# Kernel optimization log

Measured on AMD Instinct MI355X. Metric: run time of the kernel, lower is better.

The kernel has to match this reference:

```python
import jax, jax.numpy as jnp
import numpy as np

DZ, H, DH = 128, 4, 32
DC = H * DH
B, L, N = 1, 256, 256


def setup_inputs() -> dict:
    key = jax.random.key(0)
    ks = jax.random.split(key, 12)
    s = 0.02
    return {
        "z_inter": jax.random.normal(ks[0], (B, L, N, DZ), jnp.float32),
        "dist": jax.random.uniform(ks[1], (B, L, N, N), jnp.float32) * 16.0,
        "ln_g": jnp.ones((DZ,), jnp.float32),
        "ln_b": jnp.zeros((DZ,), jnp.float32),
        "Wq": jax.random.normal(ks[2], (DZ, DC), jnp.float32) * s,
        "bq": jnp.zeros((DC,), jnp.float32),
        "Wk": jax.random.normal(ks[3], (DZ, DC), jnp.float32) * s,
        "bk": jnp.zeros((DC,), jnp.float32),
        "Wv": jax.random.normal(ks[4], (DZ, DC), jnp.float32) * s,
        "bv": jnp.zeros((DC,), jnp.float32),
        "Wg": jax.random.normal(ks[5], (DZ, DC), jnp.float32) * s,
        "bg": jnp.zeros((DC,), jnp.float32),
        "Wo": jax.random.normal(ks[6], (DC, DZ), jnp.float32) * s,
        "bo": jnp.zeros((DZ,), jnp.float32),
    }


def reference(z_inter, dist, ln_g, ln_b, Wq, bq, Wk, bk, Wv, bv, Wg, bg, Wo, bo):
    # LayerNorm over channel dim (eps matches torch default 1e-5)
    mu = jnp.mean(z_inter, axis=-1, keepdims=True)
    var = jnp.mean(jnp.square(z_inter - mu), axis=-1, keepdims=True)
    z = (z_inter - mu) / jnp.sqrt(var + 1e-5) * ln_g + ln_b  # [B,L,N,DZ]

    shp = z.shape[:-1] + (H, DH)
    q = (z @ Wq + bq).reshape(shp)  # [B,L,N,H,DH]
    k = (z @ Wk + bk).reshape(shp)
    v = (z @ Wv + bv).reshape(shp)

    scalar = 1.0 / jnp.sqrt(jnp.asarray(DH, q.dtype))
    attn = jnp.einsum('blihc,bljhc->blihj', q * scalar, k)  # [B,L,N,H,N]

    # Gaussian distance coefficient applied multiplicatively pre-softmax
    coef = jnp.exp(-jnp.square(dist / 8.0) / 2.0)[:, :, :, None, :].astype(q.dtype)
    attn = attn * coef

    attn_weights = jax.nn.softmax(attn, axis=-1)
    v_avg = jnp.einsum('blihj,bljhc->blihc', attn_weights, v)  # [B,L,N,H,DH]

    gate = jax.nn.sigmoid((z @ Wg + bg).reshape(shp))
    z_com = (v_avg * gate).reshape(z.shape[:-1] + (DC,))  # [B,L,N,DC]
    return z_com @ Wo + bo  # [B,L,N,DZ]
```

## Files before the change

### kernel.cpp

```cpp
#include <hip/hip_runtime.h>
#include <hip/hip_fp16.h>

#define LDIM 256
#define NDIM 256
#define DZC  128
#define HN   4
#define DHD  32
#define DCC  128
#define MROWS (LDIM*NDIM)

typedef _Float16 f16;
typedef _Float16 f16x2 __attribute__((ext_vector_type(2)));
typedef _Float16 f16x4 __attribute__((ext_vector_type(4)));
typedef _Float16 f16x8 __attribute__((ext_vector_type(8)));
typedef __fp16   h16x2 __attribute__((ext_vector_type(2)));
typedef float    f32x4 __attribute__((ext_vector_type(4)));

#define SCAL 0.17677669529663687f
#define CEXP -0.011270992135622957f
#define CPRE 0.2550340490960039f

extern "C" __device__ _Float16 __ocml_exp2_f16(_Float16);

__device__ inline f16x2 pkrtz(float a, float b){
  h16x2 r = __builtin_amdgcn_cvt_pkrtz(a, b);
  union { h16x2 h; f16x2 f; } u; u.h = r;
  return u.f;
}

__global__ __launch_bounds__(256) void k0b_pack(
    const float* __restrict__ Wq, const float* __restrict__ Wk,
    const float* __restrict__ Wv, const float* __restrict__ Wg,
    const float* __restrict__ Wo, f16* __restrict__ w16)
{
  const float* Ws[5] = {Wq, Wk, Wv, Wg, Wo};
  const int tid = blockIdx.x * 256 + threadIdx.x;
  const int p = tid >> 14, rem = tid & 16383;
  const int e = rem & 7, lane = (rem >> 3) & 63, ksjt = rem >> 9;
  const int ks = ksjt & 3, jt = ksjt >> 2;
  const int col = jt*16 + (lane & 15);
  const int k   = ks*32 + (lane >> 4)*8 + e;
  w16[tid] = (f16)Ws[p][k*128 + col];
}

__global__ __launch_bounds__(256, 2) void k1_ln_qkvg(
    const float* __restrict__ z, const float* __restrict__ lng, const float* __restrict__ lnb,
    const f16* __restrict__ w16,
    const float* __restrict__ bq, const float* __restrict__ bk,
    const float* __restrict__ bv, const float* __restrict__ bg,
    f16* __restrict__ qb, f16* __restrict__ kbuf,
    f16* __restrict__ vbuf, f16* __restrict__ gateb)
{
  __shared__ f16 sb[4*32*136];
  f16* zl = sb;
  const int t = threadIdx.x;
  const int w = t >> 6, lane = t & 63;
  const int m = lane & 15, g = lane >> 4;
  const int row0 = blockIdx.x * 32;

  {
    const int r = t >> 3, part = t & 7;
    const float* zr = z + (size_t)(row0 + r)*DZC + part*16;
    float vals[16];
    float s = 0.f, sq = 0.f;
    #pragma unroll
    for (int i = 0; i < 4; ++i) {
      float4 v4 = reinterpret_cast<const float4*>(zr)[i];
      vals[i*4+0]=v4.x; vals[i*4+1]=v4.y; vals[i*4+2]=v4.z; vals[i*4+3]=v4.w;
      s  += v4.x+v4.y+v4.z+v4.w;
      sq += v4.x*v4.x + v4.y*v4.y + v4.z*v4.z + v4.w*v4.w;
    }
    s  += __shfl_xor(s, 1);  sq += __shfl_xor(sq, 1);
    s  += __shfl_xor(s, 2);  sq += __shfl_xor(sq, 2);
    s  += __shfl_xor(s, 4);  sq += __shfl_xor(sq, 4);
    const float mu  = s * (1.f/DZC);
    const float var = sq * (1.f/DZC) - mu*mu;
    const float rstd = rsqrtf(var + 1e-5f);
    const float* gg = lng + part*16;
    const float* bb = lnb + part*16;
    #pragma unroll
    for (int i = 0; i < 2; ++i) {
      f16x8 o;
      #pragma unroll
      for (int e = 0; e < 8; ++e)
        o[e] = (f16)((vals[i*8+e]-mu)*rstd*gg[i*8+e] + bb[i*8+e]);
      *reinterpret_cast<f16x8*>(zl + r*128 + (((part*2+i) ^ (r&7))*8)) = o;
    }
  }
  __syncthreads();

  const f16* wp = w16 + w*16384;
  f32x4 acc[2][8];
  #pragma unroll
  for (int it=0;it<2;++it)
    #pragma unroll
    for (int jt=0;jt<8;++jt) acc[it][jt] = (f32x4){0.f,0.f,0.f,0.f};

  #pragma unroll
  for (int ks = 0; ks < 4; ++ks) {
    f16x8 af[8];
    #pragma unroll
    for (int jt=0;jt<8;++jt)
      af[jt] = *reinterpret_cast<const f16x8*>(wp + ((jt*4+ks)*64 + lane)*8);
    f16x8 bf[2];
    #pragma unroll
    for (int it=0;it<2;++it)
      bf[it] = *reinterpret_cast<const f16x8*>(zl + (it*16+m)*128 + (((ks*4+g) ^ (m&7))*8));
    #pragma unroll
    for (int it=0;it<2;++it)
      #pragma unroll
      for (int jt=0;jt<8;++jt)
        acc[it][jt] = __builtin_amdgcn_mfma_f32_16x16x32_f16(af[jt], bf[it], acc[it][jt], 0,0,0);
  }

  const float* bsp = (w==0) ? bq : (w==1) ? bk : (w==2) ? bv : bg;
  float4 bias[8];
  #pragma unroll
  for (int jt=0;jt<8;++jt)
    bias[jt] = *reinterpret_cast<const float4*>(bsp + jt*16 + g*4);

  __syncthreads();

  f16* tl = sb + w*(32*136);
  #pragma unroll
  for (int it=0;it<2;++it) {
    #pragma unroll
    for (int jt=0;jt<8;++jt) {
      f16x4 o;
      #pragma unroll
      for (int r=0;r<4;++r) {
        float v = acc[it][jt][r] + ((const float*)&bias[jt])[r];
        if (w == 3) v = 1.f/(1.f + __expf(-v));
        o[r] = (f16)v;
      }
      *reinterpret_cast<f16x4*>(tl + (it*16+m)*136 + jt*16 + g*4) = o;
    }
  }
  f16* ob = (w==0) ? qb : (w==1) ? kbuf : (w==2) ? vbuf : gateb;
  #pragma unroll
  for (int p = 0; p < 8; ++p) {
    const int rr = p*4 + g, cc = m*8;
    const f16x8 v = *reinterpret_cast<const f16x8*>(tl + rr*136 + cc);
    *reinterpret_cast<f16x8*>(ob + (size_t)(row0 + rr)*DCC + cc) = v;
  }
}

__global__ __launch_bounds__(256, 2) void k2_attn(
    const f16* __restrict__ qb, const f16* __restrict__ kbuf,
    const f16* __restrict__ vbuf, const f16* __restrict__ gateb,
    const float* __restrict__ dist, const f16* __restrict__ wo16,
    const float* __restrict__ bo, float* __restrict__ out)
{
  __shared__ f16 vt[4*32*256];
  __shared__ f16 cfl[2][64*64];
  const int t = threadIdx.x;
  const int w = t >> 6, lane = t & 63;
  const int m = lane & 15, g = lane >> 4;
  const int orig = blockIdx.x;
  const int swz = (orig & 7)*64 + (orig >> 3);
  const int l = swz >> 1, half = swz & 1;
  const int r0 = half*128;
  const int lrow0 = l*NDIM;

  {
    #pragma unroll
    for (int hh = 0; hh < 4; ++hh) {
      const f16* vr = vbuf + (size_t)(lrow0 + t)*DCC + hh*DHD;
      #pragma unroll
      for (int p = 0; p < 4; ++p) {
        f16x8 v = *reinterpret_cast<const f16x8*>(vr + p*8);
        #pragma unroll
        for (int e = 0; e < 8; ++e) {
          const int c = p*8 + e;
          vt[hh*8192 + c*256 + (((t>>2) ^ (c&15))*4) + (t&3)] = v[e];
        }
      }
    }
  }

  f16x8 aq[8];
  #pragma unroll
  for (int it = 0; it < 8; ++it)
    aq[it] = *reinterpret_cast<const f16x8*>(
        qb + (size_t)(lrow0 + r0 + it*16 + m)*DCC + w*DHD + g*8);

  f32x4 o[8][2];
  float rs[8];
  #pragma unroll
  for (int it = 0; it < 8; ++it) {
    o[it][0] = (f32x4){0.f,0.f,0.f,0.f};
    o[it][1] = (f32x4){0.f,0.f,0.f,0.f};
    rs[it] = 0.f;
  }

  const float* drow = dist + (size_t)l*(NDIM*NDIM);
  const int prow[4] = { (0*256+t) >> 4, (1*256+t) >> 4, (2*256+t) >> 4, (3*256+t) >> 4 };
  const int pf4  = t & 15;

  float4 pf[4];
  #pragma unroll
  for (int p = 0; p < 4; ++p)
    pf[p] = *reinterpret_cast<const float4*>(
        drow + (size_t)(r0 + prow[p])*NDIM + pf4*4);

  __syncthreads();

  const f16* vth = vt + w*8192;

  #pragma unroll 1
  for (int jc = 0; jc < 4; ++jc) {
    f16x8 kf[4];
    #pragma unroll
    for (int jt = 0; jt < 4; ++jt)
      kf[jt] = *reinterpret_cast<const f16x8*>(
          kbuf + (size_t)(lrow0 + jc*64 + jt*16 + m)*DCC + w*DHD + g*8);

    f16x8 bvv[2][2];
    #pragma unroll
    for (int kc = 0; kc < 2; ++kc)
      #pragma unroll
      for (int ct = 0; ct < 2; ++ct) {
        const int c = ct*16 + m;
        const f16x4 lo = *reinterpret_cast<const f16x4*>(
            vth + c*256 + (((jc*16 + (2*kc+0)*4 + g) ^ m) * 4));
        const f16x4 hi = *reinterpret_cast<const f16x4*>(
            vth + c*256 + (((jc*16 + (2*kc+1)*4 + g) ^ m) * 4));
        f16x8 bb;
        #pragma unroll
        for (int e = 0; e < 4; ++e) { bb[e] = lo[e]; bb[4+e] = hi[e]; }
        bvv[kc][ct] = bb;
      }

    #pragma unroll
    for (int rh = 0; rh < 2; ++rh) {
      f16* cflc = &cfl[rh][0];
      {
        const float4 dd[4] = {pf[0], pf[1], pf[2], pf[3]};
        #pragma unroll
        for (int p = 0; p < 4; ++p) {
          const int row = prow[p];
          const f16x2 a = pkrtz(CPRE*exp2f(dd[p].x*dd[p].x*CEXP),
                                CPRE*exp2f(dd[p].y*dd[p].y*CEXP));
          const f16x2 b = pkrtz(CPRE*exp2f(dd[p].z*dd[p].z*CEXP),
                                CPRE*exp2f(dd[p].w*dd[p].w*CEXP));
          const f16x4 cf = __builtin_shufflevector(a, b, 0,1,2,3);
          *reinterpret_cast<f16x4*>(cflc + row*64 + ((pf4 ^ (row & 15))*4)) = cf;
        }
      }
      {
        const int si1 = jc*2 + rh + 1;
        const int sic = (si1 > 7) ? 7 : si1;
        const int jn = sic >> 1, rn = sic & 1;
        #pragma unroll
        for (int p = 0; p < 4; ++p)
          pf[p] = *reinterpret_cast<const float4*>(
              drow + (size_t)(r0 + rn*64 + prow[p])*NDIM + jn*64 + pf4*4);
      }
      __syncthreads();

      #pragma unroll
      for (int itl = 0; itl < 4; ++itl) {
        const int it = rh*4 + itl;
        const int lr = itl*16 + m;
        f16x4 cl[4];
        #pragma unroll
        for (int jt = 0; jt < 4; ++jt)
          cl[jt] = *reinterpret_cast<const f16x4*>(
              cflc + lr*64 + (((jt*4 + g) ^ m)*4));

        f32x4 s[4];
        #pragma unroll
        for (int jt = 0; jt < 4; ++jt)
          s[jt] = __builtin_amdgcn_mfma_f32_16x16x32_f16(
              kf[jt], aq[it], (f32x4){0.f,0.f,0.f,0.f}, 0, 0, 0);

        f16x4 pkk[4];
        #pragma unroll
        for (int jt = 0; jt < 4; ++jt) {
          const f16x2 sl = pkrtz(s[jt][0], s[jt][1]);
          const f16x2 sh = pkrtz(s[jt][2], s[jt][3]);
          const f16x2 cll = __builtin_shufflevector(cl[jt], cl[jt], 0,1);
          const f16x2 clh = __builtin_shufflevector(cl[jt], cl[jt], 2,3);
          const f16x2 xl = sl * cll;
          const f16x2 xh = sh * clh;
          f16x4 pv;
          pv[0] = __ocml_exp2_f16(xl[0]);
          pv[1] = __ocml_exp2_f16(xl[1]);
          pv[2] = __ocml_exp2_f16(xh[0]);
          pv[3] = __ocml_exp2_f16(xh[1]);
          pkk[jt] = pv;
        }
        {
          const f16x4 ps4 = (pkk[0] + pkk[1]) + (pkk[2] + pkk[3]);
          const f16x2 ps2 = __builtin_shufflevector(ps4, ps4, 0,1)
                          + __builtin_shufflevector(ps4, ps4, 2,3);
          rs[it] += (float)ps2[0] + (float)ps2[1];
        }

        #pragma unroll
        for (int kc = 0; kc < 2; ++kc) {
          const f16x8 ap = __builtin_shufflevector(pkk[2*kc], pkk[2*kc+1],
                                                   0,1,2,3,4,5,6,7);
          o[it][0] = __builtin_amdgcn_mfma_f32_16x16x32_f16(ap, bvv[kc][0], o[it][0], 0, 0, 0);
          o[it][1] = __builtin_amdgcn_mfma_f32_16x16x32_f16(ap, bvv[kc][1], o[it][1], 0, 0, 0);
        }
      }
    }
  }

  float rinv[8];
  #pragma unroll
  for (int it = 0; it < 8; ++it) {
    float v = rs[it];
    v += __shfl_xor(v, 16);
    v += __shfl_xor(v, 32);
    rinv[it] = 1.f / v;
  }

  __syncthreads();
  f16* zc = vt;
  #pragma unroll
  for (int it = 0; it < 8; ++it)
    #pragma unroll
    for (int r = 0; r < 4; ++r) {
      const float rr = __shfl(rinv[it], (lane & 48) + g*4 + r);
      const int lrow = it*16 + g*4 + r;
      #pragma unroll
      for (int ct = 0; ct < 2; ++ct)
        zc[lrow*132 + w*DHD + ct*16 + m] = (f16)(o[it][ct][r] * rr);
    }
  __syncthreads();

  f32x4 acc2[2][8];
  #pragma unroll
  for (int it2=0;it2<2;++it2)
    #pragma unroll
    for (int jt=0;jt<8;++jt) acc2[it2][jt] = (f32x4){0.f,0.f,0.f,0.f};

  #pragma unroll
  for (int ks = 0; ks < 4; ++ks) {
    f16x8 af[8];
    #pragma unroll
    for (int jt=0;jt<8;++jt)
      af[jt] = *reinterpret_cast<const f16x8*>(wo16 + ((jt*4+ks)*64 + lane)*8);
    f16x8 bf[2];
    #pragma unroll
    for (int it2 = 0; it2 < 2; ++it2) {
      const int lrow = w*32 + it2*16 + m;
      const f16x4 b0 = *reinterpret_cast<const f16x4*>(zc + lrow*132 + ks*32 + g*8);
      const f16x4 b1 = *reinterpret_cast<const f16x4*>(zc + lrow*132 + ks*32 + g*8 + 4);
      const f16x8 zf = __builtin_shufflevector(b0, b1, 0,1,2,3,4,5,6,7);
      const f16x8 gf = *reinterpret_cast<const f16x8*>(
          gateb + (size_t)(lrow0 + r0 + lrow)*DCC + ks*32 + g*8);
      bf[it2] = zf * gf;
    }
    #pragma unroll
    for (int it2=0;it2<2;++it2)
      #pragma unroll
      for (int jt=0;jt<8;++jt)
        acc2[it2][jt] = __builtin_amdgcn_mfma_f32_16x16x32_f16(af[jt], bf[it2], acc2[it2][jt], 0,0,0);
  }

  #pragma unroll
  for (int it2 = 0; it2 < 2; ++it2) {
    const size_t grow = (size_t)(lrow0 + r0 + w*32 + it2*16 + m);
    #pragma unroll
    for (int jt = 0; jt < 8; ++jt) {
      const float4 bias = *reinterpret_cast<const float4*>(bo + jt*16 + g*4);
      float4 ov;
      ov.x = acc2[it2][jt][0] + bias.x;
      ov.y = acc2[it2][jt][1] + bias.y;
      ov.z = acc2[it2][jt][2] + bias.z;
      ov.w = acc2[it2][jt][3] + bias.w;
      *reinterpret_cast<float4*>(out + grow*DZC + jt*16 + g*4) = ov;
    }
  }
}

extern "C" void kernel_launch(void* const* d_in, const int* in_sizes, int n_in,
                              void* d_out, int out_size, void* d_ws, size_t ws_size,
                              hipStream_t stream) {
  const float* z    = (const float*)d_in[0];
  const float* dist = (const float*)d_in[1];
  const float* lng  = (const float*)d_in[2];
  const float* lnb  = (const float*)d_in[3];
  const float* Wq   = (const float*)d_in[4];
  const float* bq   = (const float*)d_in[5];
  const float* Wk   = (const float*)d_in[6];
  const float* bk   = (const float*)d_in[7];
  const float* Wv   = (const float*)d_in[8];
  const float* bv   = (const float*)d_in[9];
  const float* Wg   = (const float*)d_in[10];
  const float* bg   = (const float*)d_in[11];
  const float* Wo   = (const float*)d_in[12];
  const float* bo   = (const float*)d_in[13];
  float* out = (float*)d_out;

  const size_t elems = (size_t)MROWS * DCC;
  f16* qb    = (f16*)d_ws;
  f16* kbuf  = qb    + elems;
  f16* vbuf  = kbuf  + elems;
  f16* gateb = vbuf  + elems;
  f16* w16   = gateb + elems;

  k0b_pack<<<320, 256, 0, stream>>>(Wq, Wk, Wv, Wg, Wo, w16);
  k1_ln_qkvg<<<MROWS/32, 256, 0, stream>>>(z, lng, lnb, w16, bq, bk, bv, bg,
                                           qb, kbuf, vbuf, gateb);
  k2_attn<<<LDIM*2, 256, 0, stream>>>(qb, kbuf, vbuf, gateb, dist,
                                      w16 + 4*16384, bo, out);
}
```

Before: 76.88 us.

## Compute softmax row sums via MFMA with ones and prefetch next K chunk

The per-row softmax denominator was built from packed f16 adds, a float accumulation and cross-lane shuffles. It is now produced by an extra MFMA that multiplies the probability tile by a vector of ones, which yields the row sums already in output-fragment layout. This removes the VALU reduction and the shuffle-based broadcast of the reciprocal. K fragments for the next column chunk are also loaded one iteration early, so that global load latency overlaps compute. The cost is 50% more MFMAs in the PV stage and extra registers for the accumulators and the prefetched fragments, which may reduce occupancy.

```diff
diff --git a/kernel.cpp b/kernel.cpp
--- a/kernel.cpp
+++ b/kernel.cpp
@@ -184,13 +184,17 @@
     aq[it] = *reinterpret_cast<const f16x8*>(
         qb + (size_t)(lrow0 + r0 + it*16 + m)*DCC + w*DHD + g*8);
 
+  f16x8 ones;
+  #pragma unroll
+  for (int e = 0; e < 8; ++e) ones[e] = (f16)1.0f;
+
   f32x4 o[8][2];
-  float rs[8];
+  f32x4 rsacc[8];
   #pragma unroll
   for (int it = 0; it < 8; ++it) {
     o[it][0] = (f32x4){0.f,0.f,0.f,0.f};
     o[it][1] = (f32x4){0.f,0.f,0.f,0.f};
-    rs[it] = 0.f;
+    rsacc[it] = (f32x4){0.f,0.f,0.f,0.f};
   }
 
   const float* drow = dist + (size_t)l*(NDIM*NDIM);
@@ -202,6 +206,11 @@
   for (int p = 0; p < 4; ++p)
     pf[p] = *reinterpret_cast<const float4*>(
         drow + (size_t)(r0 + prow[p])*NDIM + pf4*4);
+  f16x8 kfc[4];
+  #pragma unroll
+  for (int jt = 0; jt < 4; ++jt)
+    kfc[jt] = *reinterpret_cast<const f16x8*>(
+        kbuf + (size_t)(lrow0 + jt*16 + m)*DCC + w*DHD + g*8);
 
   __syncthreads();
 
@@ -209,11 +218,14 @@
 
   #pragma unroll 1
   for (int jc = 0; jc < 4; ++jc) {
-    f16x8 kf[4];
-    #pragma unroll
-    for (int jt = 0; jt < 4; ++jt)
-      kf[jt] = *reinterpret_cast<const f16x8*>(
-          kbuf + (size_t)(lrow0 + jc*64 + jt*16 + m)*DCC + w*DHD + g*8);
+    f16x8 kfn[4];
+    {
+      const int jn2 = (jc + 1 > 3) ? 3 : jc + 1;
+      #pragma unroll
+      for (int jt = 0; jt < 4; ++jt)
+        kfn[jt] = *reinterpret_cast<const f16x8*>(
+            kbuf + (size_t)(lrow0 + jn2*64 + jt*16 + m)*DCC + w*DHD + g*8);
+    }
 
     f16x8 bvv[2][2];
     #pragma unroll
@@ -272,7 +284,7 @@
         #pragma unroll
         for (int jt = 0; jt < 4; ++jt)
           s[jt] = __builtin_amdgcn_mfma_f32_16x16x32_f16(
-              kf[jt], aq[it], (f32x4){0.f,0.f,0.f,0.f}, 0, 0, 0);
+              kfc[jt], aq[it], (f32x4){0.f,0.f,0.f,0.f}, 0, 0, 0);
 
         f16x4 pkk[4];
         #pragma unroll
@@ -290,12 +302,6 @@
           pv[3] = __ocml_exp2_f16(xh[1]);
           pkk[jt] = pv;
         }
-        {
-          const f16x4 ps4 = (pkk[0] + pkk[1]) + (pkk[2] + pkk[3]);
-          const f16x2 ps2 = __builtin_shufflevector(ps4, ps4, 0,1)
-                          + __builtin_shufflevector(ps4, ps4, 2,3);
-          rs[it] += (float)ps2[0] + (float)ps2[1];
-        }
 
         #pragma unroll
         for (int kc = 0; kc < 2; ++kc) {
@@ -303,19 +309,20 @@
                                                    0,1,2,3,4,5,6,7);
           o[it][0] = __builtin_amdgcn_mfma_f32_16x16x32_f16(ap, bvv[kc][0], o[it][0], 0, 0, 0);
           o[it][1] = __builtin_amdgcn_mfma_f32_16x16x32_f16(ap, bvv[kc][1], o[it][1], 0, 0, 0);
+          rsacc[it] = __builtin_amdgcn_mfma_f32_16x16x32_f16(ap, ones, rsacc[it], 0, 0, 0);
         }
       }
     }
-  }
-
-  float rinv[8];
-  #pragma unroll
-  for (int it = 0; it < 8; ++it) {
-    float v = rs[it];
-    v += __shfl_xor(v, 16);
-    v += __shfl_xor(v, 32);
-    rinv[it] = 1.f / v;
-  }
+    #pragma unroll
+    for (int jt = 0; jt < 4; ++jt) kfc[jt] = kfn[jt];
+  }
+
+  f32x4 rinv[8];
+  #pragma unroll
+  for (int it = 0; it < 8; ++it)
+    #pragma unroll
+    for (int r = 0; r < 4; ++r)
+      rinv[it][r] = 1.f / rsacc[it][r];
 
   __syncthreads();
   f16* zc = vt;
@@ -323,11 +330,10 @@
   for (int it = 0; it < 8; ++it)
     #pragma unroll
     for (int r = 0; r < 4; ++r) {
-      const float rr = __shfl(rinv[it], (lane & 48) + g*4 + r);
       const int lrow = it*16 + g*4 + r;
       #pragma unroll
       for (int ct = 0; ct < 2; ++ct)
-        zc[lrow*132 + w*DHD + ct*16 + m] = (f16)(o[it][ct][r] * rr);
+        zc[lrow*132 + w*DHD + ct*16 + m] = (f16)(o[it][ct][r] * rinv[it][r]);
     }
   __syncthreads();
 
```

Result: no change. 77.95 us (+1.4%).
